# Optimization experiments

Measured on AMD Instinct MI355X. Metric: run time of the kernel, lower is better.

The kernel has to match this reference:

```python
import jax, jax.numpy as jnp
import numpy as np

N, T, F = 4096, 24, 16          # nodes, seq_len, in_features
H = 128                          # temporal_hidden
NH, DO = 4, 32                   # gat num_heads, gat out_features (NH*DO == H)
SEM, PH = 64, 32                 # semantic hidden, predictor hidden
SLOPE = 0.2                      # leaky_relu negative slope
ADJ_P = 0.01                     # adjacency density


def setup_inputs() -> dict:
    key = jax.random.key(0)
    ks = jax.random.split(key, 40)
    f32 = jnp.float32

    def rn(k, shape, s=0.02):
        return jax.random.normal(k, shape, f32) * s

    features = jax.random.normal(ks[0], (N, T, F), f32)
    pos_adj = (jax.random.uniform(ks[1], (N, N)) < ADJ_P).astype(f32)
    neg_adj = (jax.random.uniform(ks[2], (N, N)) < ADJ_P).astype(f32)

    inp = dict(features=features, pos_adj=pos_adj, neg_adj=neg_adj)
    # GRU (torch layout: W_ih [3H,F], W_hh [3H,H], gate order r,z,n)
    inp['gru_Wih'] = rn(ks[3], (3 * H, F), 1.0 / np.sqrt(H))
    inp['gru_Whh'] = rn(ks[4], (3 * H, H), 1.0 / np.sqrt(H))
    inp['gru_bih'] = rn(ks[5], (3 * H,), 1.0 / np.sqrt(H))
    inp['gru_bhh'] = rn(ks[6], (3 * H,), 1.0 / np.sqrt(H))
    # GAT params (linear weights stored [in, out] so we use x @ W)
    i = 7
    for pre in ('pos', 'neg'):
        inp[pre + '_W'] = rn(ks[i], (H, NH * DO)); i += 1
        inp[pre + '_u'] = rn(ks[i], (NH, DO, 1), 1.0); i += 1
        inp[pre + '_v'] = rn(ks[i], (NH, DO, 1), 1.0); i += 1
        inp[pre + '_b'] = rn(ks[i], (1, NH * DO)); i += 1
        inp[pre + '_pW'] = rn(ks[i], (H, NH * DO)); i += 1
        inp[pre + '_pb'] = jnp.zeros((NH * DO,), f32)
    inp['self_W'] = rn(ks[i], (H, H)); i += 1
    inp['self_b'] = jnp.zeros((H,), f32)
    inp['mpos_W'] = rn(ks[i], (NH * DO, H)); i += 1
    inp['mpos_b'] = jnp.zeros((H,), f32)
    inp['mneg_W'] = rn(ks[i], (NH * DO, H)); i += 1
    inp['mneg_b'] = jnp.zeros((H,), f32)
    inp['sem_W1'] = rn(ks[i], (H, SEM)); i += 1
    inp['sem_b1'] = jnp.zeros((SEM,), f32)
    inp['sem_W2'] = rn(ks[i], (SEM, 1)); i += 1
    inp['pred_W1'] = rn(ks[i], (H, PH)); i += 1
    inp['pred_b1'] = jnp.zeros((PH,), f32)
    inp['pred_W2'] = rn(ks[i], (PH, 1)); i += 1
    inp['pred_b2'] = jnp.zeros((1,), f32)
    return inp


def _gru_last(x, Wih, Whh, bih, bhh):
    # x: [N, T, F] -> last hidden state [N, H]
    gi_all = jnp.einsum('ntf,gf->tng', x, Wih) + bih  # precompute input gates [T,N,3H]
    h0 = jnp.zeros((x.shape[0], Whh.shape[1]), x.dtype)

    def step(h, gi):
        gh = h @ Whh.T + bhh
        ir, iz, in_ = jnp.split(gi, 3, axis=-1)
        hr, hz, hn = jnp.split(gh, 3, axis=-1)
        r = jax.nn.sigmoid(ir + hr)
        z = jax.nn.sigmoid(iz + hz)
        n = jnp.tanh(in_ + r * hn)
        return (1.0 - z) * n + z * h, None

    h, _ = jax.lax.scan(step, h0, gi_all)
    return h


def _gat(x, adj, W, u, v, b, pW, pb):
    sup = (x @ W).reshape(-1, NH, DO).transpose(1, 0, 2)     # [NH, N, DO]
    f1 = jnp.matmul(sup, u).reshape(NH, 1, -1)               # [NH, 1, N]
    f2 = jnp.matmul(sup, v).reshape(NH, -1, 1)               # [NH, N, 1]
    w = jax.nn.leaky_relu(f1 + f2, SLOPE)                    # [NH, N, N]
    mw = w * adj                                             # mask
    rs = mw.sum(axis=2, keepdims=True)
    rs = jnp.where(rs == 0, jnp.ones_like(rs), rs)
    attn = mw / rs
    out = jnp.matmul(attn, sup).transpose(1, 0, 2).reshape(-1, NH * DO)
    return out + b + x @ pW + pb                             # bias + residual


def _pairnorm_si(x):
    x = x - x.mean(axis=0)
    rn = jnp.sqrt(1e-6 + (x * x).sum(axis=1, keepdims=True))
    return x / rn


def reference(features, pos_adj, neg_adj,
              gru_Wih, gru_Whh, gru_bih, gru_bhh,
              pos_W, pos_u, pos_v, pos_b, pos_pW, pos_pb,
              neg_W, neg_u, neg_v, neg_b, neg_pW, neg_pb,
              self_W, self_b, mpos_W, mpos_b, mneg_W, mneg_b,
              sem_W1, sem_b1, sem_W2,
              pred_W1, pred_b1, pred_W2, pred_b2):
    support = _gru_last(features, gru_Wih, gru_Whh, gru_bih, gru_bhh)  # [N, H]
    pos_sup = _gat(support, pos_adj, pos_W, pos_u, pos_v, pos_b, pos_pW, pos_pb)
    neg_sup = _gat(support, neg_adj, neg_W, neg_u, neg_v, neg_b, neg_pW, neg_pb)
    self_e = support @ self_W + self_b
    pos_e = pos_sup @ mpos_W + mpos_b
    neg_e = neg_sup @ mneg_W + mneg_b
    emb = jnp.stack([self_e, pos_e, neg_e], axis=1)          # [N, 3, H]
    w = jnp.tanh(emb @ sem_W1 + sem_b1) @ sem_W2             # [N, 3, 1]
    beta = jax.nn.softmax(w, axis=1)
    fused = (beta * emb).sum(axis=1)                          # [N, H]
    fused = _pairnorm_si(fused)
    h = jax.nn.relu(fused @ pred_W1 + pred_b1)               # dropout is eval no-op
    out = jax.nn.sigmoid(h @ pred_W2 + pred_b2).squeeze(-1)  # [N]
    return out
```

## Files before the change

kernel.cpp:

```cpp
#include <hip/hip_runtime.h>


#define NN 4096

typedef unsigned short u16;
typedef unsigned int   u32;
typedef __attribute__((ext_vector_type(8))) short  short8;
typedef __attribute__((ext_vector_type(4))) float  float4v;

__device__ inline float bf2f(u16 u){ return __uint_as_float(((u32)u)<<16); }
__device__ inline u16 f2bf(float f){
  u32 x = __float_as_uint(f);
  return (u16)((x + 0x7fffu + ((x>>16)&1u))>>16);
}
__device__ inline float ldm(const void* p, int i, int bf){
  return bf ? bf2f(((const u16*)p)[i]) : ((const float*)p)[i];
}
__device__ inline u16 ldm16(const void* p, int i, int bf){
  return bf ? ((const u16*)p)[i] : f2bf(((const float*)p)[i]);
}
__device__ inline float fexp(float x){
  x = fminf(fmaxf(x,-80.f),80.f);
  return __builtin_amdgcn_exp2f(x*1.4426950408889634f);
}
__device__ inline float sigm(float x){
  return __builtin_amdgcn_rcpf(1.f + fexp(-x));
}
__device__ inline float tanhf_(float x){
  float c = fminf(fmaxf(x,-15.f),15.f);
  float e = __builtin_amdgcn_exp2f(c*2.8853900817779268f);
  return (e-1.f)*__builtin_amdgcn_rcpf(e+1.f);
}
__device__ inline float4v mfma16(short8 a, short8 b, float4v c){
  return __builtin_amdgcn_mfma_f32_16x16x32_bf16(a,b,c,0,0,0);
}

__global__ __launch_bounds__(256) void k_detect(const u32* __restrict__ adj,
                                                int* __restrict__ mflag)
{
  int i = (blockIdx.x*256 + threadIdx.x)*4;
  uint4 v = *(const uint4*)(adj + i);
  u32 acc = (v.x | v.y | v.z | v.w) & 0xFFFFu;
  unsigned long long b = __ballot(acc != 0);
  if ((threadIdx.x & 63) == 0 && b) atomicOr(mflag, 1);
}

__global__ __launch_bounds__(256) void k_imp(
  const int* __restrict__ mflag,
  const void* gWih, const void* gWhh, const void* gbih, const void* gbhh,
  const void* posW, const void* posu, const void* posv, const void* posb,
  const void* pospW, const void* pospb,
  const void* negW, const void* negu, const void* negv, const void* negb,
  const void* negpW, const void* negpb,
  const void* selfW, const void* selfb, const void* mposW, const void* mposb,
  const void* mnegW, const void* mnegb,
  const void* semW1, const void* semb1, const void* semW2,
  const void* predW1, const void* predb1, const void* predW2, const void* predb2,
  u16* __restrict__ Wihb, u16* __restrict__ Whhb,
  u16* __restrict__ WT1,  u16* __restrict__ WT2,
  float* __restrict__ cbrz, float* __restrict__ cbin, float* __restrict__ cbhn,
  float* __restrict__ cuv,  float* __restrict__ cgb,  float* __restrict__ csb,
  float* __restrict__ cw1,  float* __restrict__ cb1,  float* __restrict__ cw2,
  float* __restrict__ cpw1, float* __restrict__ cpb1, float* __restrict__ cpw2,
  float* __restrict__ cpb2)
{
  const int bf = mflag[0];
  int i = blockIdx.x*256 + threadIdx.x;
  if (i < 6144){ Wihb[i]=ldm16(gWih,i,bf); return; }  i-=6144;
  if (i < 49152){ Whhb[i]=ldm16(gWhh,i,bf); return; } i-=49152;
  if (i < 81920){
    int m=i>>7,k=i&127,sel=m>>7,ml=m&127;
    const void* s = sel==0?posW: sel==1?pospW: sel==2?negW: sel==3?negpW: selfW;
    WT1[i]=ldm16(s,k*128+ml,bf); return;
  } i-=81920;
  if (i < 32768){
    int m=i>>7,k=i&127;
    const void* s = (m<128)? mposW : mnegW;
    WT2[i]=ldm16(s,k*128+(m&127),bf); return;
  } i-=32768;
  if (i < 256){ cbrz[i]=ldm(gbih,i,bf)+ldm(gbhh,i,bf); return; } i-=256;
  if (i < 128){ cbin[i]=ldm(gbih,256+i,bf); return; } i-=128;
  if (i < 128){ cbhn[i]=ldm(gbhh,256+i,bf); return; } i-=128;
  if (i < 512){
    int s=i>>8, rem=i&255, wh=rem>>7, hd=rem&127;
    const void* p = s? (wh? negv:negu) : (wh? posv:posu);
    cuv[i]=ldm(p,hd,bf); return;
  } i-=512;
  if (i < 256){
    int s=i>>7, d=i&127;
    cgb[i]=ldm(s?negb:posb,d,bf)+ldm(s?negpb:pospb,d,bf); return;
  } i-=256;
  if (i < 384){
    int t=i>>7, d=i&127;
    const void* p = t==0? selfb : t==1? mposb : mnegb;
    csb[i]=ldm(p,d,bf); return;
  } i-=384;
  if (i < 8192){ cw1[i]=ldm(semW1,i,bf); return; } i-=8192;
  if (i < 64){ cb1[i]=ldm(semb1,i,bf); return; } i-=64;
  if (i < 64){ cw2[i]=ldm(semW2,i,bf); return; } i-=64;
  if (i < 4096){ cpw1[i]=ldm(predW1,i,bf); return; } i-=4096;
  if (i < 32){ cpb1[i]=ldm(predb1,i,bf); return; } i-=32;
  if (i < 32){ cpw2[i]=ldm(predW2,i,bf); return; } i-=32;
  if (i < 1){ cpb2[i]=ldm(predb2,i,bf); return; }
}

__global__ __launch_bounds__(256) void k_csr(
  const int* __restrict__ mflag,
  const void* posadj, const void* negadj,
  int* __restrict__ deg, u16* __restrict__ idx)
{
  const int bf = mflag[0];
  const int s = blockIdx.y;
  const void* adj = s? negadj : posadj;
  const int row  = blockIdx.x*4 + (threadIdx.x>>6);
  const int lane = threadIdx.x&63;
  u16* out = idx + ((size_t)s*NN + row)*128;
  int total = 0;
  if (bf){
    const u16* rp = (const u16*)adj + (size_t)row*4096;
    for (int it=0; it<8; it++){
      const uint4 vv = *(const uint4*)(rp + it*512 + lane*8);
      u32 wds[4] = {vv.x, vv.y, vv.z, vv.w};
      u32 m = 0;
      #pragma unroll
      for (int q=0;q<4;q++){
        if (wds[q]&0xffffu) m |= 1u<<(2*q);
        if (wds[q]>>16)     m |= 1u<<(2*q+1);
      }
      int cnt = __popc(m);
      int pre = cnt;
      #pragma unroll
      for (int off=1; off<64; off<<=1){
        int o = __shfl_up(pre, off);
        if (lane>=off) pre += o;
      }
      int base = total + (pre - cnt);
      u32 mm = m; int k = 0;
      while (mm){
        int b = __ffs(mm)-1; mm &= mm-1;
        int p = base + k; k++;
        if (p<128) out[p] = (u16)(it*512 + lane*8 + b);
      }
      total += __shfl(pre, 63);
    }
  } else {
    const float* rp = (const float*)adj + (size_t)row*4096;
    for (int it=0; it<16; it++){
      const uint4 vv = *(const uint4*)(rp + it*256 + lane*4);
      u32 m = 0;
      if (vv.x) m|=1u; if (vv.y) m|=2u; if (vv.z) m|=4u; if (vv.w) m|=8u;
      int cnt = __popc(m);
      int pre = cnt;
      #pragma unroll
      for (int off=1; off<64; off<<=1){
        int o = __shfl_up(pre, off);
        if (lane>=off) pre += o;
      }
      int base = total + (pre - cnt);
      u32 mm = m; int k = 0;
      while (mm){
        int b = __ffs(mm)-1; mm &= mm-1;
        int p = base + k; k++;
        if (p<128) out[p] = (u16)(it*256 + lane*4 + b);
      }
      total += __shfl(pre, 63);
    }
  }
  if (lane==0) deg[s*NN+row] = total>128 ? 128 : total;
}

__global__ __launch_bounds__(256) void k_gru(
  const int* __restrict__ mflag, const void* feat,
  const u16* __restrict__ Wihb, const u16* __restrict__ Whhb,
  const float* __restrict__ cbrz, const float* __restrict__ cbin,
  const float* __restrict__ cbhn, u16* __restrict__ supb)
{
  __shared__ __attribute__((aligned(16))) u16 sh_x[16*392];
  __shared__ __attribute__((aligned(16))) u16 hbuf[2][16*136];

  const int tid=threadIdx.x, lane=tid&63, wv=tid>>6;
  const int quad=lane>>4, c15=lane&15;
  const int n0=blockIdx.x*16;
  const int bf=mflag[0];

  if (bf){
    const u16* f16p=(const u16*)feat;
    for (int i=tid;i<16*384;i+=256){ int n=i/384,e=i-n*384; sh_x[n*392+e]=f16p[(size_t)(n0+n)*384+e]; }
  } else {
    const float* f32p=(const float*)feat;
    for (int i=tid;i<16*384;i+=256){ int n=i/384,e=i-n*384; sh_x[n*392+e]=f2bf(f32p[(size_t)(n0+n)*384+e]); }
  }
  for (int i=tid;i<16*136;i+=256) hbuf[0][i]=0;

  const short8 z8={0,0,0,0,0,0,0,0};
  const float4v z4={0.f,0.f,0.f,0.f};

  short8 bh[6][4], bx[6];
  #pragma unroll
  for (int q=0;q<6;q++){
    int tile=(q>>1)*8 + 2*wv + (q&1);
    int g=tile*16+c15;
    #pragma unroll
    for (int ks=0;ks<4;ks++) bh[q][ks]=*(const short8*)(Whhb+(size_t)g*128+ks*32+quad*8);
    bx[q] = (quad<2)? *(const short8*)(Wihb+(size_t)g*16+quad*8) : z8;
  }

  const int j0=wv*32+c15, j1=j0+16;
  const float brz_r0=cbrz[j0],     brz_r1=cbrz[j1];
  const float brz_z0=cbrz[128+j0], brz_z1=cbrz[128+j1];
  const float bin0=cbin[j0], bin1=cbin[j1];
  const float bhn0=cbhn[j0], bhn1=cbhn[j1];

  float hr0[4]={0.f,0.f,0.f,0.f}, hr1[4]={0.f,0.f,0.f,0.f};

  __syncthreads();

  for (int t=0;t<24;t++){
    const u16* hb  = hbuf[t&1];
    u16*       hbn = hbuf[(t+1)&1];
    short8 ah[4];
    #pragma unroll
    for (int ks=0;ks<4;ks++) ah[ks]=*(const short8*)(hb + c15*136 + ks*32 + quad*8);
    short8 ax = (quad<2)? *(const short8*)(sh_x + c15*392 + t*16 + quad*8) : z8;

    float4v r0a = mfma16(ax,bx[0],z4);
    float4v r1a = mfma16(ax,bx[1],z4);
    float4v z0a = mfma16(ax,bx[2],z4);
    float4v z1a = mfma16(ax,bx[3],z4);
    float4v ni0 = mfma16(ax,bx[4],z4);
    float4v ni1 = mfma16(ax,bx[5],z4);
    float4v nh0 = z4, nh1 = z4;
    #pragma unroll
    for (int ks=0;ks<4;ks++){
      r0a = mfma16(ah[ks],bh[0][ks],r0a);
      r1a = mfma16(ah[ks],bh[1][ks],r1a);
      z0a = mfma16(ah[ks],bh[2][ks],z0a);
      z1a = mfma16(ah[ks],bh[3][ks],z1a);
      nh0 = mfma16(ah[ks],bh[4][ks],nh0);
      nh1 = mfma16(ah[ks],bh[5][ks],nh1);
    }
    #pragma unroll
    for (int rr=0;rr<4;rr++){
      const int node = quad*4+rr;
      float r_ = sigm(r0a[rr]+brz_r0);
      float z_ = sigm(z0a[rr]+brz_z0);
      float n_ = tanhf_(ni0[rr]+bin0 + r_*(nh0[rr]+bhn0));
      float hv = (1.f-z_)*n_ + z_*hr0[rr];
      hr0[rr]=hv; hbn[node*136+j0]=f2bf(hv);
      r_ = sigm(r1a[rr]+brz_r1);
      z_ = sigm(z1a[rr]+brz_z1);
      n_ = tanhf_(ni1[rr]+bin1 + r_*(nh1[rr]+bhn1));
      hv = (1.f-z_)*n_ + z_*hr1[rr];
      hr1[rr]=hv; hbn[node*136+j1]=f2bf(hv);
    }
    __syncthreads();
  }
  #pragma unroll
  for (int rr=0;rr<4;rr++){
    const int node=quad*4+rr;
    supb[(size_t)(n0+node)*128+j0]=f2bf(hr0[rr]);
    supb[(size_t)(n0+node)*128+j1]=f2bf(hr1[rr]);
  }
}

__global__ __launch_bounds__(256) void k_lin1(
  const u16* __restrict__ supb, const u16* __restrict__ WT1, float* __restrict__ C1)
{
  __shared__ __attribute__((aligned(16))) u16 sA[16*136];
  const int tid=threadIdx.x, lane=tid&63, wv=tid>>6, quad=lane>>4, c15=lane&15;
  const int n0=blockIdx.x*16;
  for (int i=tid;i<2048;i+=256){ int n=i>>7,k=i&127; sA[n*136+k]=supb[(size_t)(n0+n)*128+k]; }
  __syncthreads();
  short8 a[4];
  #pragma unroll
  for (int ks=0;ks<4;ks++) a[ks]=*(const short8*)(sA+c15*136+ks*32+quad*8);
  for (int q=0;q<10;q++){
    int tile=wv*10+q;
    float4v acc={0.f,0.f,0.f,0.f};
    #pragma unroll
    for (int ks=0;ks<4;ks++){
      short8 b=*(const short8*)(WT1+(size_t)(tile*16+c15)*128+ks*32+quad*8);
      acc=mfma16(a[ks],b,acc);
    }
    #pragma unroll
    for (int r=0;r<4;r++) C1[(size_t)(n0+quad*4+r)*640 + tile*16 + c15]=acc[r];
  }
}

__global__ __launch_bounds__(256) void k_f12(const float* __restrict__ C1,
  const float* __restrict__ cuv, float* __restrict__ f12)
{
  int id = blockIdx.x*256+threadIdx.x;
  int n=id&4095, h=(id>>12)&3, which=(id>>14)&1, s=id>>15;
  const float* uv = cuv + s*256 + which*128;
  const float* SL = C1 + (size_t)n*640 + s*256 + h*32;
  float t=0.f;
  #pragma unroll
  for (int d=0;d<32;d++) t += SL[d]*uv[h*32+d];
  f12[id]=t;
}

__global__ __launch_bounds__(256) void k_gat(
  const float* __restrict__ C1, const float* __restrict__ f12,
  const int* __restrict__ deg, const u16* __restrict__ idx,
  const float* __restrict__ cgb, u16* __restrict__ spnb)
{
  const int s=blockIdx.y;
  const int i=blockIdx.x*4 + (threadIdx.x>>6);
  const int lane=threadIdx.x&63;
  const int d0=lane, d1=lane+64, h0=d0>>5, h1=d1>>5;
  const float* f1 = f12 + s*32768;
  const float* f2 = f12 + s*32768 + 16384;
  const float f2v0=f2[h0*4096+i], f2v1=f2[h1*4096+i];
  const u16* nb = idx + ((size_t)s*NN+i)*128;
  const int dg = deg[s*NN+i];
  float acc0=0.f,acc1=0.f,rs0=0.f,rs1=0.f;
  for (int e=0;e<dg;e++){
    int j = nb[e];
    float w0 = f1[h0*4096+j]+f2v0; w0 = w0>0.f? w0 : 0.2f*w0;
    float w1 = f1[h1*4096+j]+f2v1; w1 = w1>0.f? w1 : 0.2f*w1;
    const float* SL = C1 + (size_t)j*640 + s*256;
    acc0 += w0*SL[d0]; acc1 += w1*SL[d1];
    rs0 += w0; rs1 += w1;
  }
  if (rs0==0.f) rs0=1.f;
  if (rs1==0.f) rs1=1.f;
  const float* P = C1 + (size_t)i*640 + s*256 + 128;
  float o0 = acc0/rs0 + cgb[s*128+d0] + P[d0];
  float o1 = acc1/rs1 + cgb[s*128+d1] + P[d1];
  size_t o = ((size_t)s*NN + i)*128;
  spnb[o+d0]=f2bf(o0); spnb[o+d1]=f2bf(o1);
}

__global__ __launch_bounds__(256) void k_lin2(
  const u16* __restrict__ spnb, const u16* __restrict__ WT2, float* __restrict__ E)
{
  const int s=blockIdx.y;
  __shared__ __attribute__((aligned(16))) u16 sA[16*136];
  const int tid=threadIdx.x, lane=tid&63, wv=tid>>6, quad=lane>>4, c15=lane&15;
  const int n0=blockIdx.x*16;
  const u16* A = spnb + (size_t)s*NN*128;
  for (int i=tid;i<2048;i+=256){ int n=i>>7,k=i&127; sA[n*136+k]=A[(size_t)(n0+n)*128+k]; }
  __syncthreads();
  short8 a[4];
  #pragma unroll
  for (int ks=0;ks<4;ks++) a[ks]=*(const short8*)(sA+c15*136+ks*32+quad*8);
  #pragma unroll
  for (int q=0;q<2;q++){
    int tile=wv*2+q;
    float4v acc={0.f,0.f,0.f,0.f};
    #pragma unroll
    for (int ks=0;ks<4;ks++){
      short8 b=*(const short8*)(WT2+(size_t)(s*128+tile*16+c15)*128+ks*32+quad*8);
      acc=mfma16(a[ks],b,acc);
    }
    #pragma unroll
    for (int r=0;r<4;r++) E[(size_t)(n0+quad*4+r)*256 + s*128 + tile*16 + c15]=acc[r];
  }
}

__global__ __launch_bounds__(256) void k_sem(
  const float* __restrict__ C1, const float* __restrict__ E,
  const float* __restrict__ csb, const float* __restrict__ cw1,
  const float* __restrict__ cb1, const float* __restrict__ cw2,
  float* __restrict__ fused)
{
  __shared__ float sW1[128*64];
  __shared__ float sW2[64];
  __shared__ float sb1[64];
  __shared__ float sE[4][3][128];
  const int tid=threadIdx.x, wv=tid>>6, lane=tid&63;
  for (int i=tid;i<8192;i+=256) sW1[i]=cw1[i];
  if (tid<64){ sW2[tid]=cw2[tid]; sb1[tid]=cb1[tid]; }
  const int n = blockIdx.x*4 + wv;
  for (int d=lane; d<128; d+=64){
    sE[wv][0][d] = C1[(size_t)n*640+512+d] + csb[d];
    sE[wv][1][d] = E[(size_t)n*256 + d]    + csb[128+d];
    sE[wv][2][d] = E[(size_t)n*256+128+d]  + csb[256+d];
  }
  __syncthreads();
  float sc[3];
  #pragma unroll
  for (int s=0;s<3;s++){
    float t = sb1[lane];
    for (int k=0;k<128;k++) t += sE[wv][s][k]*sW1[k*64+lane];
    t = tanhf_(t);
    float p = t*sW2[lane];
    #pragma unroll
    for (int off=32; off; off>>=1) p += __shfl_xor(p, off);
    sc[s]=p;
  }
  float mx = fmaxf(sc[0], fmaxf(sc[1],sc[2]));
  float e0=fexp(sc[0]-mx), e1=fexp(sc[1]-mx), e2=fexp(sc[2]-mx);
  float inv = 1.f/(e0+e1+e2);
  float b0=e0*inv, b1=e1*inv, b2=e2*inv;
  for (int d=lane; d<128; d+=64)
    fused[(size_t)n*128+d] = b0*sE[wv][0][d] + b1*sE[wv][1][d] + b2*sE[wv][2][d];
}

__global__ __launch_bounds__(256) void k_mean(const float* __restrict__ fused,
                                              float* __restrict__ mean)
{
  const int d = blockIdx.x;
  float s=0.f;
  for (int n=threadIdx.x; n<NN; n+=256) s += fused[(size_t)n*128+d];
  __shared__ float red[256];
  red[threadIdx.x]=s; __syncthreads();
  for (int o=128;o;o>>=1){ if (threadIdx.x<o) red[threadIdx.x]+=red[threadIdx.x+o]; __syncthreads(); }
  if (!threadIdx.x) mean[d]=red[0]*(1.f/4096.f);
}

__global__ __launch_bounds__(256) void k_pred(
  const float* __restrict__ fused, const float* __restrict__ mean,
  const float* __restrict__ cpw1, const float* __restrict__ cpb1,
  const float* __restrict__ cpw2, const float* __restrict__ cpb2,
  float* __restrict__ out)
{
  __shared__ float sy[4][128];
  __shared__ float sW1[128*32];
  __shared__ float sW2[32];
  const int tid=threadIdx.x, wv=tid>>6, lane=tid&63;
  for (int i=tid;i<4096;i+=256) sW1[i]=cpw1[i];
  if (tid<32) sW2[tid]=cpw2[tid];
  const int n = blockIdx.x*4 + wv;
  float x0 = fused[(size_t)n*128+lane]    - mean[lane];
  float x1 = fused[(size_t)n*128+64+lane] - mean[64+lane];
  float ss = x0*x0 + x1*x1;
  #pragma unroll
  for (int o=32;o;o>>=1) ss += __shfl_xor(ss,o);
  float ir = 1.f/sqrtf(1e-6f + ss);
  sy[wv][lane]=x0*ir; sy[wv][64+lane]=x1*ir;
  __syncthreads();
  float h=0.f;
  if (lane<32){
    h = cpb1[lane];
    for (int k=0;k<128;k++) h += sy[wv][k]*sW1[k*32+lane];
    h = h>0.f? h : 0.f;
    h = h*sW2[lane];
  }
  #pragma unroll
  for (int o=32;o;o>>=1) h += __shfl_xor(h,o);
  if (!lane){
    float z = h + cpb2[0];
    out[n] = __builtin_amdgcn_rcpf(1.f + fexp(-z));
  }
}

extern "C" void kernel_launch(void* const* d_in, const int* in_sizes, int n_in,
                              void* d_out, int out_size, void* d_ws, size_t ws_size,
                              hipStream_t stream)
{
  const void* feat  =d_in[0];
  const void* posadj=d_in[1];
  const void* negadj=d_in[2];
  const void* gWih  =d_in[3];
  const void* gWhh  =d_in[4];
  const void* gbih  =d_in[5];
  const void* gbhh  =d_in[6];
  const void* posW  =d_in[7];
  const void* posu  =d_in[8];
  const void* posv  =d_in[9];
  const void* posb  =d_in[10];
  const void* pospW =d_in[11];
  const void* pospb =d_in[12];
  const void* negW  =d_in[13];
  const void* negu  =d_in[14];
  const void* negv  =d_in[15];
  const void* negb  =d_in[16];
  const void* negpW =d_in[17];
  const void* negpb =d_in[18];
  const void* selfW =d_in[19];
  const void* selfb =d_in[20];
  const void* mposW =d_in[21];
  const void* mposb =d_in[22];
  const void* mnegW =d_in[23];
  const void* mnegb =d_in[24];
  const void* semW1 =d_in[25];
  const void* semb1 =d_in[26];
  const void* semW2 =d_in[27];
  const void* predW1=d_in[28];
  const void* predb1=d_in[29];
  const void* predW2=d_in[30];
  const void* predb2=d_in[31];

  char* wsb=(char*)d_ws; size_t off=0;
  auto alloc=[&](size_t bytes)->void*{ void* p=wsb+off; off+=(bytes+255)&~(size_t)255; return p; };
  int*   mflag=(int*)  alloc(256);
  u16*   Wihb =(u16*)  alloc(6144*2);
  u16*   Whhb =(u16*)  alloc(49152*2);
  u16*   WT1  =(u16*)  alloc(81920*2);
  u16*   WT2  =(u16*)  alloc(32768*2);
  float* cbrz =(float*)alloc(256*4);
  float* cbin =(float*)alloc(128*4);
  float* cbhn =(float*)alloc(128*4);
  float* cuv  =(float*)alloc(512*4);
  float* cgb  =(float*)alloc(256*4);
  float* csb  =(float*)alloc(384*4);
  float* cw1  =(float*)alloc(8192*4);
  float* cb1  =(float*)alloc(64*4);
  float* cw2  =(float*)alloc(64*4);
  float* cpw1 =(float*)alloc(4096*4);
  float* cpb1 =(float*)alloc(32*4);
  float* cpw2 =(float*)alloc(32*4);
  float* cpb2 =(float*)alloc(4);
  u16*   supb =(u16*)  alloc((size_t)NN*128*2);
  float* C1   =(float*)alloc((size_t)NN*640*4);
  float* f12  =(float*)alloc((size_t)65536*4);
  int*   deg  =(int*)  alloc((size_t)2*NN*4);
  u16*   nidx =(u16*)  alloc((size_t)2*NN*128*2);
  u16*   spnb =(u16*)  alloc((size_t)2*NN*128*2);
  float* E    =(float*)alloc((size_t)NN*256*4);
  float* fused=(float*)alloc((size_t)NN*128*4);
  float* mean =(float*)alloc(128*4);
  (void)ws_size; (void)in_sizes; (void)n_in; (void)out_size;

  hipMemsetAsync(mflag, 0, 4, stream);
  k_detect<<<16,             256,0,stream>>>((const u32*)posadj,mflag);
  k_imp   <<<720,            256,0,stream>>>(mflag,gWih,gWhh,gbih,gbhh,
              posW,posu,posv,posb,pospW,pospb,negW,negu,negv,negb,negpW,negpb,
              selfW,selfb,mposW,mposb,mnegW,mnegb,semW1,semb1,semW2,
              predW1,predb1,predW2,predb2,
              Wihb,Whhb,WT1,WT2,cbrz,cbin,cbhn,cuv,cgb,csb,cw1,cb1,cw2,
              cpw1,cpb1,cpw2,cpb2);
  k_csr <<<dim3(NN/4,2),     256,0,stream>>>(mflag,posadj,negadj,deg,nidx);
  k_gru <<<NN/16,            256,0,stream>>>(mflag,feat,Wihb,Whhb,cbrz,cbin,cbhn,supb);
  k_lin1<<<NN/16,            256,0,stream>>>(supb,WT1,C1);
  k_f12 <<<256,              256,0,stream>>>(C1,cuv,f12);
  k_gat <<<dim3(NN/4,2),     256,0,stream>>>(C1,f12,deg,nidx,cgb,spnb);
  k_lin2<<<dim3(NN/16,2),    256,0,stream>>>(spnb,WT2,E);
  k_sem <<<NN/4,             256,0,stream>>>(C1,E,csb,cw1,cb1,cw2,fused);
  k_mean<<<128,              256,0,stream>>>(fused,mean);
  k_pred<<<NN/4,             256,0,stream>>>(fused,mean,cpw1,cpb1,cpw2,cpb2,(float*)d_out);
}
```

Measured before the change: 324.4 us.

## Batch adjacency loads into one scan in CSR and split GRU across eight waves

The CSR builder now loads a whole adjacency row into registers at once, packs nonzeros into a 64-bit per-lane mask, and does a single wave prefix scan instead of one scan per chunk. This cuts repeated shuffle scans and serialized load latency. The GRU kernel moves from 4 waves to 8 waves per 16-node block, each wave owning 16 hidden units instead of 32. That halves per-wave MFMA work on the serial recurrence, at the cost of more waves contending for barriers and registers.

```diff
diff --git a/kernel.cpp b/kernel.cpp
--- a/kernel.cpp
+++ b/kernel.cpp
@@ -5,6 +5,7 @@
 
 typedef unsigned short u16;
 typedef unsigned int   u32;
+typedef unsigned long long u64;
 typedef __attribute__((ext_vector_type(8))) short  short8;
 typedef __attribute__((ext_vector_type(4))) float  float4v;
 
@@ -115,61 +116,55 @@
   const int row  = blockIdx.x*4 + (threadIdx.x>>6);
   const int lane = threadIdx.x&63;
   u16* out = idx + ((size_t)s*NN + row)*128;
-  int total = 0;
+  u64 mask = 0;
   if (bf){
-    const u16* rp = (const u16*)adj + (size_t)row*4096;
+    const uint4* rp = (const uint4*)((const u16*)adj + (size_t)row*4096);
+    uint4 v[8];
+    #pragma unroll
+    for (int it=0; it<8; it++) v[it] = rp[it*64 + lane];
+    #pragma unroll
     for (int it=0; it<8; it++){
-      const uint4 vv = *(const uint4*)(rp + it*512 + lane*8);
-      u32 wds[4] = {vv.x, vv.y, vv.z, vv.w};
-      u32 m = 0;
+      u32 w[4]={v[it].x,v[it].y,v[it].z,v[it].w};
       #pragma unroll
       for (int q=0;q<4;q++){
-        if (wds[q]&0xffffu) m |= 1u<<(2*q);
-        if (wds[q]>>16)     m |= 1u<<(2*q+1);
+        if (w[q]&0xffffu) mask |= 1ull<<(it*8+2*q);
+        if (w[q]>>16)     mask |= 1ull<<(it*8+2*q+1);
       }
-      int cnt = __popc(m);
-      int pre = cnt;
-      #pragma unroll
-      for (int off=1; off<64; off<<=1){
-        int o = __shfl_up(pre, off);
-        if (lane>=off) pre += o;
-      }
-      int base = total + (pre - cnt);
-      u32 mm = m; int k = 0;
-      while (mm){
-        int b = __ffs(mm)-1; mm &= mm-1;
-        int p = base + k; k++;
-        if (p<128) out[p] = (u16)(it*512 + lane*8 + b);
-      }
-      total += __shfl(pre, 63);
     }
   } else {
-    const float* rp = (const float*)adj + (size_t)row*4096;
+    const uint4* rp = (const uint4*)((const float*)adj + (size_t)row*4096);
+    uint4 v[16];
+    #pragma unroll
+    for (int it=0; it<16; it++) v[it] = rp[it*64 + lane];
+    #pragma unroll
     for (int it=0; it<16; it++){
-      const uint4 vv = *(const uint4*)(rp + it*256 + lane*4);
-      u32 m = 0;
-      if (vv.x) m|=1u; if (vv.y) m|=2u; if (vv.z) m|=4u; if (vv.w) m|=8u;
-      int cnt = __popc(m);
-      int pre = cnt;
-      #pragma unroll
-      for (int off=1; off<64; off<<=1){
-        int o = __shfl_up(pre, off);
-        if (lane>=off) pre += o;
-      }
-      int base = total + (pre - cnt);
-      u32 mm = m; int k = 0;
-      while (mm){
-        int b = __ffs(mm)-1; mm &= mm-1;
-        int p = base + k; k++;
-        if (p<128) out[p] = (u16)(it*256 + lane*4 + b);
-      }
-      total += __shfl(pre, 63);
+      if (v[it].x) mask |= 1ull<<(it*4+0);
+      if (v[it].y) mask |= 1ull<<(it*4+1);
+      if (v[it].z) mask |= 1ull<<(it*4+2);
+      if (v[it].w) mask |= 1ull<<(it*4+3);
     }
   }
+  int cnt = __popcll(mask);
+  int pre = cnt;
+  #pragma unroll
+  for (int off=1; off<64; off<<=1){
+    int o = __shfl_up(pre, off);
+    if (lane>=off) pre += o;
+  }
+  int base = pre - cnt;
+  int total = __shfl(pre, 63);
+  u64 mm = mask; int k = 0;
+  while (mm){
+    int b = __ffsll(mm)-1; mm &= mm-1;
+    int e = bf ? ((b>>3)*512 + lane*8 + (b&7))
+               : ((b>>2)*256 + lane*4 + (b&3));
+    int p = base + k; k++;
+    if (p<128) out[p] = (u16)e;
+  }
   if (lane==0) deg[s*NN+row] = total>128 ? 128 : total;
 }
 
-__global__ __launch_bounds__(256) void k_gru(
+__global__ __launch_bounds__(512) void k_gru(
   const int* __restrict__ mflag, const void* feat,
   const u16* __restrict__ Wihb, const u16* __restrict__ Whhb,
   const float* __restrict__ cbrz, const float* __restrict__ cbin,
@@ -185,33 +180,30 @@
 
   if (bf){
     const u16* f16p=(const u16*)feat;
-    for (int i=tid;i<16*384;i+=256){ int n=i/384,e=i-n*384; sh_x[n*392+e]=f16p[(size_t)(n0+n)*384+e]; }
+    for (int i=tid;i<16*384;i+=512){ int n=i/384,e=i-n*384; sh_x[n*392+e]=f16p[(size_t)(n0+n)*384+e]; }
   } else {
     const float* f32p=(const float*)feat;
-    for (int i=tid;i<16*384;i+=256){ int n=i/384,e=i-n*384; sh_x[n*392+e]=f2bf(f32p[(size_t)(n0+n)*384+e]); }
-  }
-  for (int i=tid;i<16*136;i+=256) hbuf[0][i]=0;
+    for (int i=tid;i<16*384;i+=512){ int n=i/384,e=i-n*384; sh_x[n*392+e]=f2bf(f32p[(size_t)(n0+n)*384+e]); }
+  }
+  for (int i=tid;i<16*136;i+=512) hbuf[0][i]=0;
 
   const short8 z8={0,0,0,0,0,0,0,0};
   const float4v z4={0.f,0.f,0.f,0.f};
 
-  short8 bh[6][4], bx[6];
-  #pragma unroll
-  for (int q=0;q<6;q++){
-    int tile=(q>>1)*8 + 2*wv + (q&1);
-    int g=tile*16+c15;
-    #pragma unroll
-    for (int ks=0;ks<4;ks++) bh[q][ks]=*(const short8*)(Whhb+(size_t)g*128+ks*32+quad*8);
-    bx[q] = (quad<2)? *(const short8*)(Wihb+(size_t)g*16+quad*8) : z8;
-  }
-
-  const int j0=wv*32+c15, j1=j0+16;
-  const float brz_r0=cbrz[j0],     brz_r1=cbrz[j1];
-  const float brz_z0=cbrz[128+j0], brz_z1=cbrz[128+j1];
-  const float bin0=cbin[j0], bin1=cbin[j1];
-  const float bhn0=cbhn[j0], bhn1=cbhn[j1];
-
-  float hr0[4]={0.f,0.f,0.f,0.f}, hr1[4]={0.f,0.f,0.f,0.f};
+  short8 bh[3][4], bx[3];
+  #pragma unroll
+  for (int g=0;g<3;g++){
+    int rowb=(g*8+wv)*16+c15;
+    #pragma unroll
+    for (int ks=0;ks<4;ks++) bh[g][ks]=*(const short8*)(Whhb+(size_t)rowb*128+ks*32+quad*8);
+    bx[g] = (quad<2)? *(const short8*)(Wihb+(size_t)rowb*16+quad*8) : z8;
+  }
+
+  const int j0=wv*16+c15;
+  const float brz_r=cbrz[j0], brz_z=cbrz[128+j0];
+  const float bin0=cbin[j0],  bhn0=cbhn[j0];
+
+  float hr[4]={0.f,0.f,0.f,0.f};
 
   __syncthreads();
 
@@ -223,43 +215,31 @@
     for (int ks=0;ks<4;ks++) ah[ks]=*(const short8*)(hb + c15*136 + ks*32 + quad*8);
     short8 ax = (quad<2)? *(const short8*)(sh_x + c15*392 + t*16 + quad*8) : z8;
 
-    float4v r0a = mfma16(ax,bx[0],z4);
-    float4v r1a = mfma16(ax,bx[1],z4);
-    float4v z0a = mfma16(ax,bx[2],z4);
-    float4v z1a = mfma16(ax,bx[3],z4);
-    float4v ni0 = mfma16(ax,bx[4],z4);
-    float4v ni1 = mfma16(ax,bx[5],z4);
-    float4v nh0 = z4, nh1 = z4;
+    float4v racc = mfma16(ax,bx[0],z4);
+    float4v zacc = mfma16(ax,bx[1],z4);
+    float4v ni   = mfma16(ax,bx[2],z4);
+    float4v nh   = z4;
     #pragma unroll
     for (int ks=0;ks<4;ks++){
-      r0a = mfma16(ah[ks],bh[0][ks],r0a);
-      r1a = mfma16(ah[ks],bh[1][ks],r1a);
-      z0a = mfma16(ah[ks],bh[2][ks],z0a);
-      z1a = mfma16(ah[ks],bh[3][ks],z1a);
-      nh0 = mfma16(ah[ks],bh[4][ks],nh0);
-      nh1 = mfma16(ah[ks],bh[5][ks],nh1);
+      racc = mfma16(ah[ks],bh[0][ks],racc);
+      zacc = mfma16(ah[ks],bh[1][ks],zacc);
+      nh   = mfma16(ah[ks],bh[2][ks],nh);
     }
     #pragma unroll
     for (int rr=0;rr<4;rr++){
       const int node = quad*4+rr;
-      float r_ = sigm(r0a[rr]+brz_r0);
-      float z_ = sigm(z0a[rr]+brz_z0);
-      float n_ = tanhf_(ni0[rr]+bin0 + r_*(nh0[rr]+bhn0));
-      float hv = (1.f-z_)*n_ + z_*hr0[rr];
-      hr0[rr]=hv; hbn[node*136+j0]=f2bf(hv);
-      r_ = sigm(r1a[rr]+brz_r1);
-      z_ = sigm(z1a[rr]+brz_z1);
-      n_ = tanhf_(ni1[rr]+bin1 + r_*(nh1[rr]+bhn1));
-      hv = (1.f-z_)*n_ + z_*hr1[rr];
-      hr1[rr]=hv; hbn[node*136+j1]=f2bf(hv);
+      float r_ = sigm(racc[rr]+brz_r);
+      float z_ = sigm(zacc[rr]+brz_z);
+      float n_ = tanhf_(ni[rr]+bin0 + r_*(nh[rr]+bhn0));
+      float hv = (1.f-z_)*n_ + z_*hr[rr];
+      hr[rr]=hv; hbn[node*136+j0]=f2bf(hv);
     }
     __syncthreads();
   }
   #pragma unroll
   for (int rr=0;rr<4;rr++){
     const int node=quad*4+rr;
-    supb[(size_t)(n0+node)*128+j0]=f2bf(hr0[rr]);
-    supb[(size_t)(n0+node)*128+j1]=f2bf(hr1[rr]);
+    supb[(size_t)(n0+node)*128+j0]=f2bf(hr[rr]);
   }
 }
 
@@ -523,7 +503,7 @@
               Wihb,Whhb,WT1,WT2,cbrz,cbin,cbhn,cuv,cgb,csb,cw1,cb1,cw2,
               cpw1,cpb1,cpw2,cpb2);
   k_csr <<<dim3(NN/4,2),     256,0,stream>>>(mflag,posadj,negadj,deg,nidx);
-  k_gru <<<NN/16,            256,0,stream>>>(mflag,feat,Wihb,Whhb,cbrz,cbin,cbhn,supb);
+  k_gru <<<NN/16,            512,0,stream>>>(mflag,feat,Wihb,Whhb,cbrz,cbin,cbhn,supb);
   k_lin1<<<NN/16,            256,0,stream>>>(supb,WT1,C1);
   k_f12 <<<256,              256,0,stream>>>(C1,cuv,f12);
   k_gat <<<dim3(NN/4,2),     256,0,stream>>>(C1,f12,deg,nidx,cgb,spnb);
```

Result: no change. 323.2 us (-0.4%).
